# Kernel optimization log

Measured on AMD Instinct MI355X. Metric: run time of the kernel, lower is better.

Reference implementation:

```python
import jax, jax.numpy as jnp
import numpy as np

EPS = 1e-7  # keras backend epsilon
S = 64.0
M = 0.5
B, D, NC = 1024, 512, 50000


def setup_inputs() -> dict:
    key = jax.random.key(0)
    kx, kw, kl = jax.random.split(key, 3)
    x = jax.random.normal(kx, (B, D), dtype=jnp.float32)
    W = jax.random.normal(kw, (D, NC), dtype=jnp.float32)
    labels = jax.random.randint(kl, (B,), 0, NC)
    y = jax.nn.one_hot(labels, NC, dtype=jnp.float32)  # [B, NC] one-hot targets
    return {"x": x, "y": y, "W": W}


def reference(x, y, W):
    # L2-normalize embeddings (rows) and class weights (columns)
    xn = x / jnp.linalg.norm(x, axis=1, keepdims=True)
    Wn = W / jnp.linalg.norm(W, axis=0, keepdims=True)
    logits = xn @ Wn  # [B, NC] cosine similarities
    theta = jnp.arccos(jnp.clip(logits, -1.0 + EPS, 1.0 - EPS))
    target_logits = jnp.cos(theta + M)
    logits = logits * (1.0 - y) + target_logits * y
    logits = logits * S
    return jax.nn.softmax(logits, axis=-1)
```

## Files before the change

### kernel.cpp

```cpp
#include <hip/hip_runtime.h>
#include <hip/hip_fp16.h>
#include <cstdint>
#include <cstddef>

#define NCLS 50000
#define DIM 512
#define NROW 1024
#define NTN 391

typedef _Float16 half8 __attribute__((ext_vector_type(8)));
typedef float f32x4 __attribute__((ext_vector_type(4)));

#define AS1(p) ((const __attribute__((address_space(1))) void*)(p))
#define AS3(p) ((__attribute__((address_space(3))) void*)(p))

__global__ void prep_all_kernel(const float* __restrict__ W,
                                __half* __restrict__ Wt,
                                float* __restrict__ part,
                                const float4* __restrict__ y4,
                                int* __restrict__ lab,
                                const float* __restrict__ x,
                                __half* __restrict__ xh,
                                float* __restrict__ rn)
{
    __shared__ float tile[64][65];
    __shared__ float cpart[4][64];

    const int t = threadIdx.x;
    if (blockIdx.x < 6256) {
        const int bx = blockIdx.x % 782;
        const int by = blockIdx.x / 782;
        int n0 = bx * 64;
        int k0 = by * 64;
        int f4 = t & 15;
        int kr = t >> 4;
        int n = n0 + f4 * 4;
        bool ok = (n < NCLS);
#pragma unroll
        for (int i = 0; i < 4; ++i) {
            int k = kr + i * 16;
            float4 v = ok ? *(const float4*)(W + (size_t)(k0 + k) * NCLS + n)
                          : make_float4(0.f, 0.f, 0.f, 0.f);
            tile[k][f4 * 4 + 0] = v.x;
            tile[k][f4 * 4 + 1] = v.y;
            tile[k][f4 * 4 + 2] = v.z;
            tile[k][f4 * 4 + 3] = v.w;
        }
        __syncthreads();
#pragma unroll
        for (int i = 0; i < 8; ++i) {
            int idx = t + i * 256;
            int nn = idx >> 5;
            int kp = idx & 31;
            int gn = n0 + nn;
            if (gn < NCLS) {
                __half2 h = __floats2half2_rn(tile[kp * 2][nn], tile[kp * 2 + 1][nn]);
                *(__half2*)(Wt + (size_t)gn * DIM + k0 + kp * 2) = h;
            }
        }
        {
            int nn = t & 63;
            int seg = t >> 6;
            float s = 0.f;
#pragma unroll
            for (int k = 0; k < 16; ++k) {
                float v = tile[seg * 16 + k][nn];
                s += v * v;
            }
            cpart[seg][nn] = s;
            __syncthreads();
            if (t < 64 && n0 + t < NCLS) {
                part[(size_t)by * NCLS + n0 + t] =
                    cpart[0][t] + cpart[1][t] + cpart[2][t] + cpart[3][t];
            }
        }
    } else if (blockIdx.x < 8304) {
        const int vb = blockIdx.x - 6256;
        for (int i4 = vb * 256 + t; i4 < 12800000; i4 += 2048 * 256) {
            float4 v = y4[i4];
            if (v.x != 0.f || v.y != 0.f || v.z != 0.f || v.w != 0.f) {
                long base = (long)i4 * 4;
                if (v.x != 0.f) { long i = base + 0; lab[i / NCLS] = (int)(i % NCLS); }
                if (v.y != 0.f) { long i = base + 1; lab[i / NCLS] = (int)(i % NCLS); }
                if (v.z != 0.f) { long i = base + 2; lab[i / NCLS] = (int)(i % NCLS); }
                if (v.w != 0.f) { long i = base + 3; lab[i / NCLS] = (int)(i % NCLS); }
            }
        }
    } else {
        int row = (blockIdx.x - 8304) * 4 + (t >> 6);
        int l = t & 63;
        const float4* xr = (const float4*)(x + (size_t)row * DIM);
        __half2* dst = (__half2*)(xh + (size_t)row * DIM);
        float s = 0.f;
#pragma unroll
        for (int i = 0; i < 2; ++i) {
            int idx = l + i * 64;
            float4 v = xr[idx];
            dst[idx * 2]     = __floats2half2_rn(v.x, v.y);
            dst[idx * 2 + 1] = __floats2half2_rn(v.z, v.w);
            s += v.x * v.x + v.y * v.y + v.z * v.z + v.w * v.w;
        }
#pragma unroll
        for (int off = 32; off > 0; off >>= 1) s += __shfl_down(s, off);
        if (l == 0) rn[row] = rsqrtf(s);
    }
}

__global__ void make_cn_kernel(const float* __restrict__ part, float* __restrict__ cn)
{
    int c = blockIdx.x * 256 + threadIdx.x;
    if (c >= NCLS) return;
    float s = 0.f;
#pragma unroll
    for (int j = 0; j < 8; ++j) s += part[(size_t)j * NCLS + c];
    cn[c] = rsqrtf(s);
}

template<int PASS>
__global__ __launch_bounds__(256, 4) void gemm_arc_kernel(
    const __half* __restrict__ A,
    const __half* __restrict__ Bt,
    const float* __restrict__ rn,
    const float* __restrict__ cn,
    const int* __restrict__ lab,
    const float* __restrict__ rs,
    float* __restrict__ out,
    float* __restrict__ rowpart)
{
    __shared__ __align__(16) __half As[128 * 64];
    __shared__ __align__(16) __half Bs[128 * 64];
    __shared__ float rsum[2][128];

    const int tid = threadIdx.x;
    const int wid = tid >> 6;
    const int lane = tid & 63;
    const int wm = wid >> 1;
    const int wn = wid & 1;

    const int b = blockIdx.x;
    const int w = (b & 7) * NTN + (b >> 3);
    const int mt = w & 7;
    const int nt0 = w >> 3;
    const int nt = (PASS == 1) ? (NTN - 1 - nt0) : nt0;
    const int tileM = mt * 128;
    const int tileN = nt * 128;

    const int srow = lane >> 3;
    const int sblk = (lane & 7) ^ srow;

    f32x4 acc[4][4] = {};

    auto stage = [&](int k0) {
#pragma unroll
        for (int c = 0; c < 4; ++c) {
            int chunk = wid * 4 + c;
            int row = chunk * 8 + srow;
            const __half* sa = A + (size_t)(tileM + row) * DIM + k0 + sblk * 8;
            __builtin_amdgcn_global_load_lds(AS1(sa), AS3((char*)As + chunk * 1024), 16, 0, 0);
            int gn = tileN + row;
            if (gn > NCLS - 1) gn = NCLS - 1;
            const __half* sb = Bt + (size_t)gn * DIM + k0 + sblk * 8;
            __builtin_amdgcn_global_load_lds(AS1(sb), AS3((char*)Bs + chunk * 1024), 16, 0, 0);
        }
    };

    auto compute = [&]() {
        const int krow = lane >> 4;
        const int rl = lane & 15;
#pragma unroll
        for (int kk = 0; kk < 2; ++kk) {
            half8 af[4], bf[4];
#pragma unroll
            for (int m = 0; m < 4; ++m) {
                int r = wm * 64 + m * 16 + rl;
                int kb = (kk * 4 + krow) ^ (r & 7);
                af[m] = *(const half8*)((const char*)As + r * 128 + kb * 16);
            }
#pragma unroll
            for (int n = 0; n < 4; ++n) {
                int r = wn * 64 + n * 16 + rl;
                int kb = (kk * 4 + krow) ^ (r & 7);
                bf[n] = *(const half8*)((const char*)Bs + r * 128 + kb * 16);
            }
#pragma unroll
            for (int m = 0; m < 4; ++m)
#pragma unroll
                for (int n = 0; n < 4; ++n)
                    acc[m][n] = __builtin_amdgcn_mfma_f32_16x16x32_f16(af[m], bf[n], acc[m][n], 0, 0, 0);
        }
    };

#pragma unroll 1
    for (int k0 = 0; k0 < DIM; k0 += 64) {
        stage(k0);
        __syncthreads();
        compute();
        __syncthreads();
    }

    const float cosM = 0.8775825618903728f;
    const float sinM = 0.4794255386042030f;
    const int col_l = lane & 15;
    const int rgrp = lane >> 4;
    float* buf = (float*)As;

#pragma unroll
    for (int m = 0; m < 4; ++m) {
        int lr0 = wm * 64 + m * 16 + rgrp * 4;
        int gr0 = tileM + lr0;
        float rnv[4]; int labv[4]; float rsv[4];
#pragma unroll
        for (int r = 0; r < 4; ++r) {
            rnv[r] = rn[gr0 + r];
            labv[r] = lab[gr0 + r];
            if (PASS == 1) rsv[r] = rs[gr0 + r];
        }
        float rowacc[4] = {0.f, 0.f, 0.f, 0.f};
#pragma unroll
        for (int n = 0; n < 4; ++n) {
            int gc = tileN + wn * 64 + n * 16 + col_l;
            bool okc = (gc < NCLS);
            float cnv = okc ? cn[gc] : 0.f;
#pragma unroll
            for (int r = 0; r < 4; ++r) {
                float cv = acc[m][n][r] * rnv[r] * cnv;
                float logit;
                if (gc == labv[r]) {
                    float cc = fminf(fmaxf(cv, -1.f + 1e-7f), 1.f - 1e-7f);
                    logit = 64.f * (cc * cosM - sqrtf(1.f - cc * cc) * sinM);
                } else {
                    logit = 64.f * cv;
                }
                float e = __expf(logit);
                if (PASS == 0) {
                    if (okc) rowacc[r] += e;
                } else {
                    buf[(wm * 16 + rgrp * 4 + r) * 128 + wn * 64 + n * 16 + col_l] = e * rsv[r];
                }
            }
        }
        if (PASS == 0) {
#pragma unroll
            for (int r = 0; r < 4; ++r) {
                float s = rowacc[r];
                s += __shfl_xor(s, 1);
                s += __shfl_xor(s, 2);
                s += __shfl_xor(s, 4);
                s += __shfl_xor(s, 8);
                if (col_l == 0) rsum[wn][lr0 + r] = s;
            }
        } else {
            __syncthreads();
#pragma unroll
            for (int i = 0; i < 4; ++i) {
                int idx = tid + i * 256;
                int lr = idx >> 5;
                int c4 = idx & 31;
                int gr = tileM + (lr >> 4) * 64 + m * 16 + (lr & 15);
                int gcl = tileN + c4 * 4;
                if (gcl < NCLS)
                    *(float4*)(out + (size_t)gr * NCLS + gcl) = ((float4*)buf)[idx];
            }
            __syncthreads();
        }
    }
    if (PASS == 0) {
        __syncthreads();
        if (tid < 128) {
            float tot = rsum[0][tid] + rsum[1][tid];
            rowpart[(size_t)nt * NROW + tileM + tid] = tot;
        }
    }
}

__global__ void reduce_rs_kernel(const float* __restrict__ rowpart, float* __restrict__ rs)
{
    int row = blockIdx.x * 256 + threadIdx.x;
    float s = 0.f;
    for (int t = 0; t < NTN; ++t) s += rowpart[(size_t)t * NROW + row];
    rs[row] = 1.f / s;
}

extern "C" void kernel_launch(void* const* d_in, const int* in_sizes, int n_in,
                              void* d_out, int out_size, void* d_ws, size_t ws_size,
                              hipStream_t stream)
{
    const float* x = (const float*)d_in[0];
    const float* y = (const float*)d_in[1];
    const float* W = (const float*)d_in[2];
    float* out = (float*)d_out;

    char* ws = (char*)d_ws;
    __half* Wt     = (__half*)(ws);
    __half* xh     = (__half*)(ws + 51200000);
    float* rn      = (float*) (ws + 52248576);
    float* cn      = (float*) (ws + 52252672);
    float* part    = (float*) (ws + 52452672);
    float* rowpart = part;
    int*   lab     = (int*)   (ws + 54054208);
    float* rs      = (float*) (ws + 54058304);

    hipLaunchKernelGGL(prep_all_kernel, dim3(6256 + 2048 + 256), dim3(256), 0, stream,
                       W, Wt, part, (const float4*)y, lab, x, xh, rn);
    hipLaunchKernelGGL(make_cn_kernel, dim3(196), dim3(256), 0, stream, part, cn);
    hipLaunchKernelGGL(gemm_arc_kernel<0>, dim3(8 * NTN), dim3(256), 0, stream,
                       xh, Wt, rn, cn, lab, rs, out, rowpart);
    hipLaunchKernelGGL(reduce_rs_kernel, dim3(4), dim3(256), 0, stream, rowpart, rs);
    hipLaunchKernelGGL(gemm_arc_kernel<1>, dim3(8 * NTN), dim3(256), 0, stream,
                       xh, Wt, rn, cn, lab, rs, out, rowpart);
}
```

Measured before the change: 249.3 us.

## Store bf16 exponentials in first pass and normalize in a streaming finalize kernel

```diff
diff --git a/kernel.cpp b/kernel.cpp
--- a/kernel.cpp
+++ b/kernel.cpp
@@ -10,6 +10,8 @@
 
 typedef _Float16 half8 __attribute__((ext_vector_type(8)));
 typedef float f32x4 __attribute__((ext_vector_type(4)));
+typedef unsigned short us4 __attribute__((ext_vector_type(4)));
+typedef unsigned short us8 __attribute__((ext_vector_type(8)));
 
 #define AS1(p) ((const __attribute__((address_space(1))) void*)(p))
 #define AS3(p) ((__attribute__((address_space(3))) void*)(p))
@@ -114,6 +116,184 @@
 #pragma unroll
     for (int j = 0; j < 8; ++j) s += part[(size_t)j * NCLS + c];
     cn[c] = rsqrtf(s);
+}
+
+__global__ __launch_bounds__(256, 4) void gemm_arc_e_kernel(
+    const __half* __restrict__ A,
+    const __half* __restrict__ Bt,
+    const float* __restrict__ rn,
+    const float* __restrict__ cn,
+    const int* __restrict__ lab,
+    unsigned short* __restrict__ eh,
+    float* __restrict__ rowpart)
+{
+    __shared__ __align__(16) __half As[128 * 64];
+    __shared__ __align__(16) __half Bs[128 * 64];
+    __shared__ float rsum[2][128];
+
+    const int tid = threadIdx.x;
+    const int wid = tid >> 6;
+    const int lane = tid & 63;
+    const int wm = wid >> 1;
+    const int wn = wid & 1;
+
+    const int b = blockIdx.x;
+    const int w = (b & 7) * NTN + (b >> 3);
+    const int mt = w & 7;
+    const int nt = w >> 3;
+    const int tileM = mt * 128;
+    const int tileN = nt * 128;
+
+    const int srow = lane >> 3;
+    const int sblk = (lane & 7) ^ srow;
+
+    f32x4 acc[4][4] = {};
+
+    auto stage = [&](int k0) {
+#pragma unroll
+        for (int c = 0; c < 4; ++c) {
+            int chunk = wid * 4 + c;
+            int row = chunk * 8 + srow;
+            const __half* sa = A + (size_t)(tileM + row) * DIM + k0 + sblk * 8;
+            __builtin_amdgcn_global_load_lds(AS1(sa), AS3((char*)As + chunk * 1024), 16, 0, 0);
+            int gn = tileN + row;
+            if (gn > NCLS - 1) gn = NCLS - 1;
+            const __half* sb = Bt + (size_t)gn * DIM + k0 + sblk * 8;
+            __builtin_amdgcn_global_load_lds(AS1(sb), AS3((char*)Bs + chunk * 1024), 16, 0, 0);
+        }
+    };
+
+    auto compute = [&]() {
+        const int krow = lane >> 4;
+        const int rl = lane & 15;
+#pragma unroll
+        for (int kk = 0; kk < 2; ++kk) {
+            half8 af[4], bf[4];
+#pragma unroll
+            for (int m = 0; m < 4; ++m) {
+                int r = wm * 64 + m * 16 + rl;
+                int kb = (kk * 4 + krow) ^ (r & 7);
+                af[m] = *(const half8*)((const char*)As + r * 128 + kb * 16);
+            }
+#pragma unroll
+            for (int n = 0; n < 4; ++n) {
+                int r = wn * 64 + n * 16 + rl;
+                int kb = (kk * 4 + krow) ^ (r & 7);
+                bf[n] = *(const half8*)((const char*)Bs + r * 128 + kb * 16);
+            }
+#pragma unroll
+            for (int m = 0; m < 4; ++m)
+#pragma unroll
+                for (int n = 0; n < 4; ++n)
+                    acc[m][n] = __builtin_amdgcn_mfma_f32_16x16x32_f16(af[m], bf[n], acc[m][n], 0, 0, 0);
+        }
+    };
+
+#pragma unroll 1
+    for (int k0 = 0; k0 < DIM; k0 += 64) {
+        stage(k0);
+        __syncthreads();
+        compute();
+        __syncthreads();
+    }
+
+    const float cosM = 0.8775825618903728f;
+    const float sinM = 0.4794255386042030f;
+    const int col_l = lane & 15;
+    const int rgrp = lane >> 4;
+    float* buf = (float*)As;
+
+#pragma unroll
+    for (int m = 0; m < 4; ++m) {
+        int lr0 = wm * 64 + m * 16 + rgrp * 4;
+        int gr0 = tileM + lr0;
+        float rnv[4]; int labv[4];
+#pragma unroll
+        for (int r = 0; r < 4; ++r) {
+            rnv[r] = rn[gr0 + r];
+            labv[r] = lab[gr0 + r];
+        }
+        float rowacc[4] = {0.f, 0.f, 0.f, 0.f};
+#pragma unroll
+        for (int n = 0; n < 4; ++n) {
+            int gc = tileN + wn * 64 + n * 16 + col_l;
+            bool okc = (gc < NCLS);
+            float cnv = okc ? cn[gc] : 0.f;
+#pragma unroll
+            for (int r = 0; r < 4; ++r) {
+                float cv = acc[m][n][r] * rnv[r] * cnv;
+                float logit;
+                if (gc == labv[r]) {
+                    float cc = fminf(fmaxf(cv, -1.f + 1e-7f), 1.f - 1e-7f);
+                    logit = 64.f * (cc * cosM - sqrtf(1.f - cc * cc) * sinM);
+                } else {
+                    logit = 64.f * cv;
+                }
+                float e = __expf(logit);
+                unsigned int u = __float_as_uint(e);
+                u += 0x7FFFu + ((u >> 16) & 1u);
+                float ef = __uint_as_float(u & 0xFFFF0000u);
+                if (okc) rowacc[r] += ef;
+                buf[(wm * 16 + rgrp * 4 + r) * 128 + wn * 64 + n * 16 + col_l] = ef;
+            }
+        }
+#pragma unroll
+        for (int r = 0; r < 4; ++r) {
+            float s = rowacc[r];
+            s += __shfl_xor(s, 1);
+            s += __shfl_xor(s, 2);
+            s += __shfl_xor(s, 4);
+            s += __shfl_xor(s, 8);
+            if (col_l == 0) rsum[wn][lr0 + r] = s;
+        }
+        __syncthreads();
+#pragma unroll
+        for (int i = 0; i < 4; ++i) {
+            int idx = tid + i * 256;
+            int lr = idx >> 5;
+            int c4 = idx & 31;
+            int gr = tileM + (lr >> 4) * 64 + m * 16 + (lr & 15);
+            int gcl = tileN + c4 * 4;
+            if (gcl < NCLS) {
+                f32x4 v = ((const f32x4*)buf)[idx];
+                us4 o;
+                o[0] = (unsigned short)(__float_as_uint(v[0]) >> 16);
+                o[1] = (unsigned short)(__float_as_uint(v[1]) >> 16);
+                o[2] = (unsigned short)(__float_as_uint(v[2]) >> 16);
+                o[3] = (unsigned short)(__float_as_uint(v[3]) >> 16);
+                *(us4*)(eh + (size_t)gr * NCLS + gcl) = o;
+            }
+        }
+        __syncthreads();
+    }
+    if (tid < 128) {
+        float tot = rsum[0][tid] + rsum[1][tid];
+        rowpart[(size_t)nt * NROW + tileM + tid] = tot;
+    }
+}
+
+__global__ void finalize_e_kernel(const unsigned short* __restrict__ eh,
+                                  const float* __restrict__ rs,
+                                  float* __restrict__ out)
+{
+    int row = blockIdx.y;
+    int i = blockIdx.x * 256 + threadIdx.x;
+    if (i < 6250) {
+        float s = rs[row];
+        us8 v = *(const us8*)(eh + (size_t)row * NCLS + i * 8);
+        float4 o0, o1;
+        o0.x = __uint_as_float((unsigned int)v[0] << 16) * s;
+        o0.y = __uint_as_float((unsigned int)v[1] << 16) * s;
+        o0.z = __uint_as_float((unsigned int)v[2] << 16) * s;
+        o0.w = __uint_as_float((unsigned int)v[3] << 16) * s;
+        o1.x = __uint_as_float((unsigned int)v[4] << 16) * s;
+        o1.y = __uint_as_float((unsigned int)v[5] << 16) * s;
+        o1.z = __uint_as_float((unsigned int)v[6] << 16) * s;
+        o1.w = __uint_as_float((unsigned int)v[7] << 16) * s;
+        float* p = out + (size_t)row * NCLS + i * 8;
+        *(float4*)p = o0;
+        *(float4*)(p + 4) = o1;
+    }
 }
 
 template<int PASS>
@@ -299,13 +479,25 @@
     float* rowpart = part;
     int*   lab     = (int*)   (ws + 54054208);
     float* rs      = (float*) (ws + 54058304);
+    unsigned short* eh = (unsigned short*)(ws + 54062400);
+
+    const size_t need = 54062400ull + 102400000ull;
 
     hipLaunchKernelGGL(prep_all_kernel, dim3(6256 + 2048 + 256), dim3(256), 0, stream,
                        W, Wt, part, (const float4*)y, lab, x, xh, rn);
     hipLaunchKernelGGL(make_cn_kernel, dim3(196), dim3(256), 0, stream, part, cn);
-    hipLaunchKernelGGL(gemm_arc_kernel<0>, dim3(8 * NTN), dim3(256), 0, stream,
-                       xh, Wt, rn, cn, lab, rs, out, rowpart);
-    hipLaunchKernelGGL(reduce_rs_kernel, dim3(4), dim3(256), 0, stream, rowpart, rs);
-    hipLaunchKernelGGL(gemm_arc_kernel<1>, dim3(8 * NTN), dim3(256), 0, stream,
-                       xh, Wt, rn, cn, lab, rs, out, rowpart);
-}
+
+    if (ws_size >= need) {
+        hipLaunchKernelGGL(gemm_arc_e_kernel, dim3(8 * NTN), dim3(256), 0, stream,
+                           xh, Wt, rn, cn, lab, eh, rowpart);
+        hipLaunchKernelGGL(reduce_rs_kernel, dim3(4), dim3(256), 0, stream, rowpart, rs);
+        hipLaunchKernelGGL(finalize_e_kernel, dim3(25, NROW), dim3(256), 0, stream,
+                           eh, rs, out);
+    } else {
+        hipLaunchKernelGGL(gemm_arc_kernel<0>, dim3(8 * NTN), dim3(256), 0, stream,
+                           xh, Wt, rn, cn, lab, rs, out, rowpart);
+        hipLaunchKernelGGL(reduce_rs_kernel, dim3(4), dim3(256), 0, stream, rowpart, rs);
+        hipLaunchKernelGGL(gemm_arc_kernel<1>, dim3(8 * NTN), dim3(256), 0, stream,
+                           xh, Wt, rn, cn, lab, rs, out, rowpart);
+    }
+}
```

After: 246.6 us. Within noise of the previous version (-1.1%).

## Store bf16 exponentials in output buffer and rescale in-place instead of recomputing GEMM

Applied to the files above, without the earlier changes.

```diff
diff --git a/kernel.cpp b/kernel.cpp
--- a/kernel.cpp
+++ b/kernel.cpp
@@ -10,6 +10,8 @@
 
 typedef _Float16 half8 __attribute__((ext_vector_type(8)));
 typedef float f32x4 __attribute__((ext_vector_type(4)));
+typedef unsigned short us4 __attribute__((ext_vector_type(4)));
+typedef unsigned short us8 __attribute__((ext_vector_type(8)));
 
 #define AS1(p) ((const __attribute__((address_space(1))) void*)(p))
 #define AS3(p) ((__attribute__((address_space(3))) void*)(p))
@@ -116,15 +118,13 @@
     cn[c] = rsqrtf(s);
 }
 
-template<int PASS>
-__global__ __launch_bounds__(256, 4) void gemm_arc_kernel(
+__global__ __launch_bounds__(256, 4) void gemm_arc_e_kernel(
     const __half* __restrict__ A,
     const __half* __restrict__ Bt,
     const float* __restrict__ rn,
     const float* __restrict__ cn,
     const int* __restrict__ lab,
-    const float* __restrict__ rs,
-    float* __restrict__ out,
+    unsigned short* __restrict__ eh,
     float* __restrict__ rowpart)
 {
     __shared__ __align__(16) __half As[128 * 64];
@@ -140,8 +140,7 @@
     const int b = blockIdx.x;
     const int w = (b & 7) * NTN + (b >> 3);
     const int mt = w & 7;
-    const int nt0 = w >> 3;
-    const int nt = (PASS == 1) ? (NTN - 1 - nt0) : nt0;
+    const int nt = w >> 3;
     const int tileM = mt * 128;
     const int tileN = nt * 128;
 
@@ -208,12 +207,11 @@
     for (int m = 0; m < 4; ++m) {
         int lr0 = wm * 64 + m * 16 + rgrp * 4;
         int gr0 = tileM + lr0;
-        float rnv[4]; int labv[4]; float rsv[4];
+        float rnv[4]; int labv[4];
 #pragma unroll
         for (int r = 0; r < 4; ++r) {
             rnv[r] = rn[gr0 + r];
             labv[r] = lab[gr0 + r];
-            if (PASS == 1) rsv[r] = rs[gr0 + r];
         }
         float rowacc[4] = {0.f, 0.f, 0.f, 0.f};
 #pragma unroll
@@ -232,44 +230,45 @@
                     logit = 64.f * cv;
                 }
                 float e = __expf(logit);
-                if (PASS == 0) {
-                    if (okc) rowacc[r] += e;
-                } else {
-                    buf[(wm * 16 + rgrp * 4 + r) * 128 + wn * 64 + n * 16 + col_l] = e * rsv[r];
-                }
-            }
-        }
-        if (PASS == 0) {
-#pragma unroll
-            for (int r = 0; r < 4; ++r) {
-                float s = rowacc[r];
-                s += __shfl_xor(s, 1);
-                s += __shfl_xor(s, 2);
-                s += __shfl_xor(s, 4);
-                s += __shfl_xor(s, 8);
-                if (col_l == 0) rsum[wn][lr0 + r] = s;
-            }
-        } else {
-            __syncthreads();
-#pragma unroll
-            for (int i = 0; i < 4; ++i) {
-                int idx = tid + i * 256;
-                int lr = idx >> 5;
-                int c4 = idx & 31;
-                int gr = tileM + (lr >> 4) * 64 + m * 16 + (lr & 15);
-                int gcl = tileN + c4 * 4;
-                if (gcl < NCLS)
-                    *(float4*)(out + (size_t)gr * NCLS + gcl) = ((float4*)buf)[idx];
-            }
-            __syncthreads();
-        }
-    }
-    if (PASS == 0) {
-        __syncthreads();
-        if (tid < 128) {
-            float tot = rsum[0][tid] + rsum[1][tid];
-            rowpart[(size_t)nt * NROW + tileM + tid] = tot;
-        }
+                unsigned int u = __float_as_uint(e);
+                u += 0x7FFFu + ((u >> 16) & 1u);
+                float ef = __uint_as_float(u & 0xFFFF0000u);
+                if (okc) rowacc[r] += ef;
+                buf[(wm * 16 + rgrp * 4 + r) * 128 + wn * 64 + n * 16 + col_l] = ef;
+            }
+        }
+#pragma unroll
+        for (int r = 0; r < 4; ++r) {
+            float s = rowacc[r];
+            s += __shfl_xor(s, 1);
+            s += __shfl_xor(s, 2);
+            s += __shfl_xor(s, 4);
+            s += __shfl_xor(s, 8);
+            if (col_l == 0) rsum[wn][lr0 + r] = s;
+        }
+        __syncthreads();
+#pragma unroll
+        for (int i = 0; i < 4; ++i) {
+            int idx = tid + i * 256;
+            int lr = idx >> 5;
+            int c4 = idx & 31;
+            int gr = tileM + (lr >> 4) * 64 + m * 16 + (lr & 15);
+            int gcl = tileN + c4 * 4;
+            if (gcl < NCLS) {
+                f32x4 v = ((const f32x4*)buf)[idx];
+                us4 o;
+                o[0] = (unsigned short)(__float_as_uint(v[0]) >> 16);
+                o[1] = (unsigned short)(__float_as_uint(v[1]) >> 16);
+                o[2] = (unsigned short)(__float_as_uint(v[2]) >> 16);
+                o[3] = (unsigned short)(__float_as_uint(v[3]) >> 16);
+                *(us4*)(eh + (size_t)gr * NCLS + gcl) = o;
+            }
+        }
+        __syncthreads();
+    }
+    if (tid < 128) {
+        float tot = rsum[0][tid] + rsum[1][tid];
+        rowpart[(size_t)nt * NROW + tileM + tid] = tot;
     }
 }
 
@@ -281,6 +280,64 @@
     rs[row] = 1.f / s;
 }
 
+__global__ void fin_stage_kernel(const unsigned short* __restrict__ eh,
+                                 const float* __restrict__ rs,
+                                 float* __restrict__ out,
+                                 int base)
+{
+    int row = base + blockIdx.y;
+    int i = blockIdx.x * 256 + threadIdx.x;
+    if (i < 6250) {
+        float s = rs[row];
+        us8 v = *(const us8*)(eh + (size_t)row * NCLS + i * 8);
+        float4 o0, o1;
+        o0.x = __uint_as_float((unsigned int)v[0] << 16) * s;
+        o0.y = __uint_as_float((unsigned int)v[1] << 16) * s;
+        o0.z = __uint_as_float((unsigned int)v[2] << 16) * s;
+        o0.w = __uint_as_float((unsigned int)v[3] << 16) * s;
+        o1.x = __uint_as_float((unsigned int)v[4] << 16) * s;
+        o1.y = __uint_as_float((unsigned int)v[5] << 16) * s;
+        o1.z = __uint_as_float((unsigned int)v[6] << 16) * s;
+        o1.w = __uint_as_float((unsigned int)v[7] << 16) * s;
+        float* p = out + (size_t)row * NCLS + i * 8;
+        *(float4*)p = o0;
+        *(float4*)(p + 4) = o1;
+    }
+}
+
+__global__ void tail_copy_kernel(const unsigned short* __restrict__ eh,
+                                 us8* __restrict__ scratch)
+{
+    int row = blockIdx.y;
+    int i = blockIdx.x * 256 + threadIdx.x;
+    if (i < 6250)
+        scratch[(size_t)row * 6250 + i] = *(const us8*)(eh + (size_t)row * NCLS + i * 8);
+}
+
+__global__ void tail_expand_kernel(const us8* __restrict__ scratch,
+                                   const float* __restrict__ rs,
+                                   float* __restrict__ out)
+{
+    int row = blockIdx.y;
+    int i = blockIdx.x * 256 + threadIdx.x;
+    if (i < 6250) {
+        float s = rs[row];
+        us8 v = scratch[(size_t)row * 6250 + i];
+        float4 o0, o1;
+        o0.x = __uint_as_float((unsigned int)v[0] << 16) * s;
+        o0.y = __uint_as_float((unsigned int)v[1] << 16) * s;
+        o0.z = __uint_as_float((unsigned int)v[2] << 16) * s;
+        o0.w = __uint_as_float((unsigned int)v[3] << 16) * s;
+        o1.x = __uint_as_float((unsigned int)v[4] << 16) * s;
+        o1.y = __uint_as_float((unsigned int)v[5] << 16) * s;
+        o1.z = __uint_as_float((unsigned int)v[6] << 16) * s;
+        o1.w = __uint_as_float((unsigned int)v[7] << 16) * s;
+        float* p = out + (size_t)row * NCLS + i * 8;
+        *(float4*)p = o0;
+        *(float4*)(p + 4) = o1;
+    }
+}
+
 extern "C" void kernel_launch(void* const* d_in, const int* in_sizes, int n_in,
                               void* d_out, int out_size, void* d_ws, size_t ws_size,
                               hipStream_t stream)
@@ -289,6 +346,7 @@
     const float* y = (const float*)d_in[1];
     const float* W = (const float*)d_in[2];
     float* out = (float*)d_out;
+    unsigned short* eh = (unsigned short*)d_out;
 
     char* ws = (char*)d_ws;
     __half* Wt     = (__half*)(ws);
@@ -299,13 +357,19 @@
     float* rowpart = part;
     int*   lab     = (int*)   (ws + 54054208);
     float* rs      = (float*) (ws + 54058304);
+    us8* scratch   = (us8*)Wt;
 
     hipLaunchKernelGGL(prep_all_kernel, dim3(6256 + 2048 + 256), dim3(256), 0, stream,
                        W, Wt, part, (const float4*)y, lab, x, xh, rn);
     hipLaunchKernelGGL(make_cn_kernel, dim3(196), dim3(256), 0, stream, part, cn);
-    hipLaunchKernelGGL(gemm_arc_kernel<0>, dim3(8 * NTN), dim3(256), 0, stream,
-                       xh, Wt, rn, cn, lab, rs, out, rowpart);
+    hipLaunchKernelGGL(gemm_arc_e_kernel, dim3(8 * NTN), dim3(256), 0, stream,
+                       xh, Wt, rn, cn, lab, eh, rowpart);
     hipLaunchKernelGGL(reduce_rs_kernel, dim3(4), dim3(256), 0, stream, rowpart, rs);
-    hipLaunchKernelGGL(gemm_arc_kernel<1>, dim3(8 * NTN), dim3(256), 0, stream,
-                       xh, Wt, rn, cn, lab, rs, out, rowpart);
-}
+    hipLaunchKernelGGL(fin_stage_kernel, dim3(25, 512), dim3(256), 0, stream, eh, rs, out, 512);
+    hipLaunchKernelGGL(fin_stage_kernel, dim3(25, 256), dim3(256), 0, stream, eh, rs, out, 256);
+    hipLaunchKernelGGL(fin_stage_kernel, dim3(25, 128), dim3(256), 0, stream, eh, rs, out, 128);
+    hipLaunchKernelGGL(fin_stage_kernel, dim3(25, 64), dim3(256), 0, stream, eh, rs, out, 64);
+    hipLaunchKernelGGL(fin_stage_kernel, dim3(25, 32), dim3(256), 0, stream, eh, rs, out, 32);
+    hipLaunchKernelGGL(tail_copy_kernel, dim3(25, 32), dim3(256), 0, stream, eh, scratch);
+    hipLaunchKernelGGL(tail_expand_kernel, dim3(25, 32), dim3(256), 0, stream, scratch, rs, out);
+}
```

Result: slower. 266.0 us (+6.7%).
